# Kernel optimization log

Measured on AMD Instinct MI355X. Metric: run time of the kernel, lower is better.

The kernel has to match this reference:

```python
import jax, jax.numpy as jnp
import numpy as np

N, K, C, S = 32768, 16, 64, 8
EPS = 1e-5

def _bn(x, g, b):
    # BatchNorm1d in training mode: normalize over all axes except channel (last)
    axes = tuple(range(x.ndim - 1))
    m = x.mean(axes, keepdims=True)
    v = x.var(axes, keepdims=True)
    return (x - m) * jax.lax.rsqrt(v + EPS) * g + b

def setup_inputs() -> dict:
    key = jax.random.key(0)
    ks = jax.random.split(key, 24)
    def W(k, i, o):
        return (jax.random.normal(k, (i, o), jnp.float32) * 0.02)
    d = {}
    d['xyz'] = jax.random.normal(ks[0], (N, 3), jnp.float32)
    d['features'] = jax.random.normal(ks[1], (N, C), jnp.float32)
    d['velocities'] = jax.random.normal(ks[2], (N, 1), jnp.float32)
    # q/k/v projections
    d['wq'] = W(ks[3], C, C); d['bq'] = jnp.zeros((C,), jnp.float32)
    d['wk'] = W(ks[4], C, C); d['bk'] = jnp.zeros((C,), jnp.float32)
    d['wv'] = W(ks[5], C, C); d['bv'] = jnp.zeros((C,), jnp.float32)
    # linear_p: Linear(3,3) -> BN(3) -> ReLU -> Linear(3,C)
    d['p1_w'] = W(ks[6], 3, 3); d['p1_b'] = jnp.zeros((3,), jnp.float32)
    d['p_bn_g'] = jnp.ones((3,), jnp.float32); d['p_bn_b'] = jnp.zeros((3,), jnp.float32)
    d['p2_w'] = W(ks[7], 3, C); d['p2_b'] = jnp.zeros((C,), jnp.float32)
    # velocity encoder: Linear(1,1) -> BN(1) -> ReLU -> Linear(1,C)
    d['v1_w'] = W(ks[8], 1, 1); d['v1_b'] = jnp.zeros((1,), jnp.float32)
    d['v_bn_g'] = jnp.ones((1,), jnp.float32); d['v_bn_b'] = jnp.zeros((1,), jnp.float32)
    d['v2_w'] = W(ks[9], 1, C); d['v2_b'] = jnp.zeros((C,), jnp.float32)
    # linear_w: BN(C) -> ReLU -> Linear(C, C//S) -> BN(C//S) -> ReLU -> Linear(C//S, C//S)
    d['w_bn1_g'] = jnp.ones((C,), jnp.float32); d['w_bn1_b'] = jnp.zeros((C,), jnp.float32)
    d['w1_w'] = W(ks[10], C, C // S); d['w1_b'] = jnp.zeros((C // S,), jnp.float32)
    d['w_bn2_g'] = jnp.ones((C // S,), jnp.float32); d['w_bn2_b'] = jnp.zeros((C // S,), jnp.float32)
    d['w2_w'] = W(ks[11], C // S, C // S); d['w2_b'] = jnp.zeros((C // S,), jnp.float32)
    # rho: BN(C) -> ReLU -> Linear(C, C)
    d['rho_bn_g'] = jnp.ones((C,), jnp.float32); d['rho_bn_b'] = jnp.zeros((C,), jnp.float32)
    d['rho_w'] = W(ks[12], C, C); d['rho_b'] = jnp.zeros((C,), jnp.float32)
    # precomputed KNN neighbor indices (coordinate-space and velocity-space)
    d['idx'] = jax.random.randint(ks[13], (N, K), 0, N, jnp.int32)
    d['idx_v'] = jax.random.randint(ks[14], (N, K), 0, N, jnp.int32)
    return d

def reference(xyz, features, velocities, wq, bq, wk, bk, wv, bv,
              p1_w, p1_b, p_bn_g, p_bn_b, p2_w, p2_b,
              v1_w, v1_b, v_bn_g, v_bn_b, v2_w, v2_b,
              w_bn1_g, w_bn1_b, w1_w, w1_b, w_bn2_g, w_bn2_b, w2_w, w2_b,
              rho_bn_g, rho_bn_b, rho_w, rho_b, idx, idx_v):
    x_q = features @ wq + bq                      # [N,C]
    x_k = features @ wk + bk
    x_v = features @ wv + bv
    # queryandgroup: gather neighbors; relative coords prepended for k-path
    p_r = xyz[idx] - xyz[:, None, :]              # [N,K,3]
    x_k_g = x_k[idx]                              # [N,K,C]
    x_v_g = x_v[idx]                              # [N,K,C]
    # positional encoder
    p_enc = jax.nn.relu(_bn(p_r @ p1_w + p1_b, p_bn_g, p_bn_b)) @ p2_w + p2_b   # [N,K,C]
    # velocity encoder (KNN in velocity space)
    v_g = velocities[idx_v]                        # [N,K,1]
    v_enc = jax.nn.relu(_bn(v_g @ v1_w + v1_b, v_bn_g, v_bn_b)) @ v2_w + v2_b   # [N,K,C]
    # subtraction attention scoring
    w = x_k_g - x_q[:, None, :] + (p_enc + v_enc)  # [N,K,C]
    w = jax.nn.relu(_bn(w, w_bn1_g, w_bn1_b)) @ w1_w + w1_b
    w = jax.nn.relu(_bn(w, w_bn2_g, w_bn2_b)) @ w2_w + w2_b   # [N,K,C//S]
    w = jax.nn.softmax(w, axis=1)                  # softmax over neighbors
    # grouped weighted sum with share_planes
    a = (x_v_g + p_enc + v_enc).reshape(N, K, S, C // S)
    out = (a * w[:, :, None, :]).sum(axis=1).reshape(N, C)
    out = out + features
    out = jax.nn.relu(_bn(out, rho_bn_g, rho_bn_b)) @ rho_w + rho_b
    return out
```

## Files before the change

### kernel.cpp

```cpp
#include <hip/hip_runtime.h>

#define NPTS 32768
#define KNN 16
#define CH 64
#define CS 8
#define NKP (NPTS*KNN)
#define EPSBN 1e-5f

#define G1 1024
#define G2 1024
#define G3 1024
#define G4 1024
#define G5 1024

struct EncParams {
  float q00,q01,q02,q10,q11,q12,q20,q21,q22;
  float pb0,pb1,pb2;
  float ps0,ps1,ps2, pt0,pt1,pt2;
  float v1w, v1b, vs, vt;
};

__device__ __forceinline__ EncParams load_enc(const float* __restrict__ p1w, const float* __restrict__ p1b,
                                              const float* __restrict__ v1w, const float* __restrict__ v1b,
                                              const float* __restrict__ stats) {
  EncParams P;
  P.q00=p1w[0]; P.q01=p1w[1]; P.q02=p1w[2];
  P.q10=p1w[3]; P.q11=p1w[4]; P.q12=p1w[5];
  P.q20=p1w[6]; P.q21=p1w[7]; P.q22=p1w[8];
  P.pb0=p1b[0]; P.pb1=p1b[1]; P.pb2=p1b[2];
  P.ps0=stats[0]; P.ps1=stats[1]; P.ps2=stats[2];
  P.pt0=stats[3]; P.pt1=stats[4]; P.pt2=stats[5];
  P.v1w=v1w[0]; P.v1b=v1b[0]; P.vs=stats[6]; P.vt=stats[7];
  return P;
}

__device__ __forceinline__ void enc_scalars(const EncParams& P, const float* __restrict__ xyz,
                                            const float* __restrict__ vel, int m, int mv,
                                            float xn0, float xn1, float xn2,
                                            float& ry0, float& ry1, float& ry2, float& rv) {
  float pr0 = xyz[m*3+0]-xn0, pr1 = xyz[m*3+1]-xn1, pr2 = xyz[m*3+2]-xn2;
  float y0 = pr0*P.q00 + pr1*P.q10 + pr2*P.q20 + P.pb0;
  float y1 = pr0*P.q01 + pr1*P.q11 + pr2*P.q21 + P.pb1;
  float y2 = pr0*P.q02 + pr1*P.q12 + pr2*P.q22 + P.pb2;
  ry0 = fmaxf(y0*P.ps0+P.pt0, 0.f);
  ry1 = fmaxf(y1*P.ps1+P.pt1, 0.f);
  ry2 = fmaxf(y2*P.ps2+P.pt2, 0.f);
  float vr = vel[mv]*P.v1w + P.v1b;
  rv = fmaxf(vr*P.vs+P.vt, 0.f);
}

__global__ __launch_bounds__(256) void k1_qkv_stats(
    const float* __restrict__ feat,
    const float* __restrict__ wq, const float* __restrict__ bq,
    const float* __restrict__ wk, const float* __restrict__ bk,
    const float* __restrict__ wv, const float* __restrict__ bv,
    const float* __restrict__ xyz, const float* __restrict__ vel,
    const float* __restrict__ p1w, const float* __restrict__ p1b,
    const float* __restrict__ v1w, const float* __restrict__ v1b,
    const int* __restrict__ idx, const int* __restrict__ idxv,
    float* __restrict__ xq, float* __restrict__ xk, float* __restrict__ xv,
    float* __restrict__ part1)
{
  __shared__ float4 lw4[3072];
  __shared__ float lf[2048];
  __shared__ float red1[32];
  float* lw = (float*)lw4;
  int tid = threadIdx.x;
  for (int i = tid; i < 3072; i += 256) {
    float4 v;
    if (i < 1024) v = ((const float4*)wq)[i];
    else if (i < 2048) v = ((const float4*)wk)[i-1024];
    else v = ((const float4*)wv)[i-2048];
    lw4[i] = v;
  }
  __syncthreads();
  int lane = tid & 63, wave = tid >> 6;
  int nb = blockIdx.x*32 + wave*8;
  #pragma unroll
  for (int r=0;r<8;r++)
    lf[wave*512 + r*64 + lane] = feat[(nb+r)*64 + lane];
  float aq[8], ak[8], av[8];
  #pragma unroll
  for (int r=0;r<8;r++){ aq[r]=0.f; ak[r]=0.f; av[r]=0.f; }
  for (int i=0;i<64;i++){
    float wqi = lw[i*64+lane];
    float wki = lw[4096+i*64+lane];
    float wvi = lw[8192+i*64+lane];
    #pragma unroll
    for (int r=0;r<8;r++){
      float f = lf[wave*512 + r*64 + i];
      aq[r] += f*wqi; ak[r] += f*wki; av[r] += f*wvi;
    }
  }
  float bql=bq[lane], bkl=bk[lane], bvl=bv[lane];
  #pragma unroll
  for (int r=0;r<8;r++){
    int row = nb + r;
    xq[row*64+lane] = aq[r]+bql;
    xk[row*64+lane] = ak[r]+bkl;
    xv[row*64+lane] = av[r]+bvl;
  }
  float q00=p1w[0],q01=p1w[1],q02=p1w[2],q10=p1w[3],q11=p1w[4],q12=p1w[5],q20=p1w[6],q21=p1w[7],q22=p1w[8];
  float pb0=p1b[0],pb1=p1b[1],pb2=p1b[2];
  float v1w_=v1w[0], v1b_=v1b[0];
  float s0=0,s1=0,s2=0,sv=0,t0=0,t1=0,t2=0,tv=0;
  int gid = blockIdx.x*256 + tid;
  #pragma unroll
  for (int rep=0; rep<2; rep++){
    int p = gid + rep*(G1*256);
    int n = p >> 4;
    int m = idx[p], mv = idxv[p];
    float xn0=xyz[n*3], xn1=xyz[n*3+1], xn2=xyz[n*3+2];
    float pr0=xyz[m*3]-xn0, pr1=xyz[m*3+1]-xn1, pr2=xyz[m*3+2]-xn2;
    float y0 = pr0*q00+pr1*q10+pr2*q20+pb0;
    float y1 = pr0*q01+pr1*q11+pr2*q21+pb1;
    float y2 = pr0*q02+pr1*q12+pr2*q22+pb2;
    float vr = vel[mv]*v1w_ + v1b_;
    s0+=y0; s1+=y1; s2+=y2; sv+=vr;
    t0+=y0*y0; t1+=y1*y1; t2+=y2*y2; tv+=vr*vr;
  }
  #pragma unroll
  for (int msk=1; msk<64; msk<<=1){
    s0 += __shfl_xor(s0,msk); s1 += __shfl_xor(s1,msk); s2 += __shfl_xor(s2,msk); sv += __shfl_xor(sv,msk);
    t0 += __shfl_xor(t0,msk); t1 += __shfl_xor(t1,msk); t2 += __shfl_xor(t2,msk); tv += __shfl_xor(tv,msk);
  }
  if (lane==0){
    red1[wave*8+0]=s0; red1[wave*8+1]=s1; red1[wave*8+2]=s2; red1[wave*8+3]=sv;
    red1[wave*8+4]=t0; red1[wave*8+5]=t1; red1[wave*8+6]=t2; red1[wave*8+7]=tv;
  }
  __syncthreads();
  if (tid < 8){
    float a = red1[tid] + red1[8+tid] + red1[16+tid] + red1[24+tid];
    part1[blockIdx.x*8 + tid] = a;
  }
}

__global__ __launch_bounds__(1024) void r1_finalize(
    const float* __restrict__ P, const float* __restrict__ pg, const float* __restrict__ pb,
    const float* __restrict__ vg, const float* __restrict__ vb, float* __restrict__ stats)
{
  constexpr int COLG = 2, NSL = 1024/COLG, ITER = G1/NSL;
  __shared__ float4 red[1024];
  int t = threadIdx.x; int cg = t % COLG, sl = t / COLG;
  float4 acc = make_float4(0.f,0.f,0.f,0.f);
  const float4* P4 = (const float4*)P;
  #pragma unroll
  for (int j=0;j<ITER;j++){
    int i = sl + j*NSL;
    float4 v = P4[i*COLG + cg];
    acc.x+=v.x; acc.y+=v.y; acc.z+=v.z; acc.w+=v.w;
  }
  red[t] = acc; __syncthreads();
  for (int off = NSL/2; off>0; off>>=1){
    if (sl < off){
      float4 o = red[(sl+off)*COLG + cg];
      acc.x+=o.x; acc.y+=o.y; acc.z+=o.z; acc.w+=o.w;
      red[sl*COLG + cg] = acc;
    }
    __syncthreads();
  }
  if (t<4){
    float s = ((float*)red)[t];
    float q = ((float*)red)[4+t];
    float inv = 1.f/(float)NKP;
    float mean=s*inv, var=q*inv-mean*mean;
    float g = (t<3)? pg[t]:vg[0];
    float b = (t<3)? pb[t]:vb[0];
    float sc = g*rsqrtf(var+EPSBN);
    float sh = b - mean*sc;
    if (t<3){ stats[t]=sc; stats[3+t]=sh; } else { stats[6]=sc; stats[7]=sh; }
  }
}

__global__ __launch_bounds__(256) void k1b_renc(
    const float* __restrict__ xyz, const float* __restrict__ vel,
    const float* __restrict__ p1w, const float* __restrict__ p1b,
    const float* __restrict__ v1w, const float* __restrict__ v1b,
    const int* __restrict__ idx, const int* __restrict__ idxv,
    const float* __restrict__ stats, float* __restrict__ renc)
{
  EncParams P = load_enc(p1w,p1b,v1w,v1b,stats);
  int p = blockIdx.x*256 + threadIdx.x;
  int n = p >> 4;
  int m = idx[p], mv = idxv[p];
  float ry0,ry1,ry2,rv;
  enc_scalars(P, xyz, vel, m, mv, xyz[n*3], xyz[n*3+1], xyz[n*3+2], ry0,ry1,ry2,rv);
  ((float4*)renc)[p] = make_float4(ry0,ry1,ry2,rv);
}

template<int NB, int NCH>
__global__ __launch_bounds__(1024) void finalize_bn_t(
    const float* __restrict__ P, float inv,
    const float* __restrict__ g, const float* __restrict__ b,
    float* __restrict__ oscale, float* __restrict__ oshift)
{
  constexpr int COLS = 2*NCH;
  constexpr int COLG = COLS/4;
  constexpr int NSL  = 1024/COLG;
  constexpr int ITER = NB/NSL;
  __shared__ float4 red[1024];
  int t = threadIdx.x; int cg = t % COLG, sl = t / COLG;
  float4 acc = make_float4(0.f,0.f,0.f,0.f);
  const float4* P4 = (const float4*)P;
  #pragma unroll 8
  for (int j=0;j<ITER;j++){
    int i = sl + j*NSL;
    float4 v = P4[i*COLG + cg];
    acc.x+=v.x; acc.y+=v.y; acc.z+=v.z; acc.w+=v.w;
  }
  red[t] = acc; __syncthreads();
  for (int off = NSL/2; off>0; off>>=1){
    if (sl < off){
      float4 o = red[(sl+off)*COLG + cg];
      acc.x+=o.x; acc.y+=o.y; acc.z+=o.z; acc.w+=o.w;
      red[sl*COLG + cg] = acc;
    }
    __syncthreads();
  }
  if (t < NCH){
    float s = ((float*)red)[t];
    float q = ((float*)red)[NCH + t];
    float mean=s*inv, var=q*inv-mean*mean;
    float sc=g[t]*rsqrtf(var+EPSBN);
    oscale[t]=sc; oshift[t]=b[t]-mean*sc;
  }
}

__global__ __launch_bounds__(256) void k2_wstats(
    const int* __restrict__ idx, const float* __restrict__ renc,
    const float* __restrict__ p2w, const float* __restrict__ p2b,
    const float* __restrict__ v2w, const float* __restrict__ v2b,
    const float* __restrict__ xq, const float* __restrict__ xk,
    float* __restrict__ part2)
{
  int tid = threadIdx.x;
  int lane = tid & 63, wave = tid >> 6;
  float A = p2w[lane], B = p2w[64+lane], C2 = p2w[128+lane];
  float D = v2w[lane], E = p2b[lane] + v2b[lane];
  const float4* renc4 = (const float4*)renc;
  float sum=0.f, ssq=0.f;
  int gw = blockIdx.x*4 + wave;
  for (int n0 = gw; n0 < NPTS; n0 += G2*4){
    int nu = __builtin_amdgcn_readfirstlane(n0);
    float xqc = xq[nu*64+lane];
    #pragma unroll 4
    for (int k=0;k<KNN;k++){
      int pu = nu*KNN + k;
      int m = idx[pu];
      float4 rr = renc4[pu];
      float e = rr.x*A + rr.y*B + rr.z*C2 + rr.w*D + E;
      float w = xk[m*64+lane] - xqc + e;
      sum += w; ssq += w*w;
    }
  }
  __shared__ float rs[4][64], rq[4][64];
  rs[wave][lane]=sum; rq[wave][lane]=ssq;
  __syncthreads();
  if (tid < 64){
    float s = rs[0][tid]+rs[1][tid]+rs[2][tid]+rs[3][tid];
    float q = rq[0][tid]+rq[1][tid]+rq[2][tid]+rq[3][tid];
    part2[blockIdx.x*128 + tid] = s;
    part2[blockIdx.x*128 + 64 + tid] = q;
  }
}

__global__ __launch_bounds__(256) void k3_w1(
    const float* __restrict__ p2w, const float* __restrict__ p2b,
    const float* __restrict__ v2w, const float* __restrict__ v2b,
    const float* __restrict__ w1w, const float* __restrict__ w1b,
    const int* __restrict__ idx, const float* __restrict__ renc,
    const float* __restrict__ xq, const float* __restrict__ xk,
    const float* __restrict__ stats,
    float* __restrict__ w1o, float* __restrict__ part3)
{
  __shared__ __attribute__((aligned(16))) float coef[64*20];
  __shared__ float rs[256], rq[256];
  int tid=threadIdx.x;
  if (tid < 64){
    int c = tid;
    int slot = ((c&7)<<3) | (c>>3);
    float* cf = &coef[slot*20];
    cf[0]=p2w[c]; cf[1]=p2w[64+c]; cf[2]=p2w[128+c];
    cf[3]=v2w[c]; cf[4]=p2b[c]+v2b[c];
    cf[5]=stats[8+c]; cf[6]=stats[72+c];
    #pragma unroll
    for (int j=0;j<8;j++) cf[7+j]=w1w[c*8+j];
    #pragma unroll
    for (int j=15;j<20;j++) cf[j]=0.f;
  }
  __syncthreads();
  int lane=tid&63, wave=tid>>6;
  int sl = lane&7, sp = lane>>3;
  float w1b_l = w1b[sl];
  const float4* renc4=(const float4*)renc;
  const float4* xk4=(const float4*)xk;
  const float4* xq4=(const float4*)xq;
  float ssum=0.f, sqq=0.f;
  int gw = blockIdx.x*4 + wave;
  for (int it = gw; it < NKP/32; it += G3*4){
    int pbase = it*32 + sp*4;
    int n = pbase >> 4;
    int4 mi = *(const int4*)&idx[pbase];
    float4 rr0 = renc4[pbase+0], rr1 = renc4[pbase+1],
           rr2 = renc4[pbase+2], rr3 = renc4[pbase+3];
    float4 xqa = xq4[n*16 + sl*2], xqb = xq4[n*16 + sl*2 + 1];
    float xqv[8] = {xqa.x,xqa.y,xqa.z,xqa.w, xqb.x,xqb.y,xqb.z,xqb.w};
    float xkv[4][8];
    {
      int mm[4] = {mi.x, mi.y, mi.z, mi.w};
      #pragma unroll
      for (int u=0;u<4;u++){
        float4 a = xk4[mm[u]*16 + sl*2], b = xk4[mm[u]*16 + sl*2 + 1];
        xkv[u][0]=a.x; xkv[u][1]=a.y; xkv[u][2]=a.z; xkv[u][3]=a.w;
        xkv[u][4]=b.x; xkv[u][5]=b.y; xkv[u][6]=b.z; xkv[u][7]=b.w;
      }
    }
    float h[4][8];
    #pragma unroll
    for (int u=0;u<4;u++)
      #pragma unroll
      for (int j=0;j<8;j++) h[u][j]=0.f;
    float4 rrs[4] = {rr0,rr1,rr2,rr3};
    #pragma unroll
    for (int r=0;r<8;r++){
      const float* cf = &coef[(r*8+sl)*20];
      float4 ca = *(const float4*)(cf+0);
      float4 cb = *(const float4*)(cf+4);
      float4 cc = *(const float4*)(cf+8);
      float4 cd = *(const float4*)(cf+12);
      #pragma unroll
      for (int u=0;u<4;u++){
        float e = rrs[u].x*ca.x + rrs[u].y*ca.y + rrs[u].z*ca.z + rrs[u].w*ca.w + cb.x;
        float w = xkv[u][r] - xqv[r] + e;
        float rw = fmaxf(w*cb.y + cb.z, 0.f);
        h[u][0] += rw*cb.w; h[u][1] += rw*cc.x; h[u][2] += rw*cc.y; h[u][3] += rw*cc.z;
        h[u][4] += rw*cc.w; h[u][5] += rw*cd.x; h[u][6] += rw*cd.y; h[u][7] += rw*cd.z;
      }
    }
    bool k1b_ = (sl&1)==0, k2b = (sl&2)==0, k4b = (sl&4)==0;
    #pragma unroll
    for (int u=0;u<4;u++){
      float a0 = k1b_? h[u][0]:h[u][1], o0 = k1b_? h[u][1]:h[u][0];
      float a1 = k1b_? h[u][2]:h[u][3], o1 = k1b_? h[u][3]:h[u][2];
      float a2 = k1b_? h[u][4]:h[u][5], o2 = k1b_? h[u][5]:h[u][4];
      float a3 = k1b_? h[u][6]:h[u][7], o3 = k1b_? h[u][7]:h[u][6];
      float g0 = a0 + __shfl_xor(o0,1);
      float g1 = a1 + __shfl_xor(o1,1);
      float g2 = a2 + __shfl_xor(o2,1);
      float g3 = a3 + __shfl_xor(o3,1);
      float b0 = k2b? g0:g1, p0 = k2b? g1:g0;
      float b1 = k2b? g2:g3, p1 = k2b? g3:g2;
      float f0 = b0 + __shfl_xor(p0,2);
      float f1 = b1 + __shfl_xor(p1,2);
      float c0 = k4b? f0:f1, q0 = k4b? f1:f0;
      float S = c0 + __shfl_xor(q0,4);
      float o = S + w1b_l;
      w1o[(pbase+u)*8 + sl] = o;
      ssum += o; sqq += o*o;
    }
  }
  rs[tid]=ssum; rq[tid]=sqq;
  __syncthreads();
  if (tid < 8){
    float s=0.f,q=0.f;
    #pragma unroll 8
    for (int i=0;i<32;i++){ s+=rs[i*8+tid]; q+=rq[i*8+tid]; }
    part3[blockIdx.x*16 + tid] = s;
    part3[blockIdx.x*16 + 8 + tid] = q;
  }
}

__global__ __launch_bounds__(256) void k4_agg(
    const float* __restrict__ feat,
    const float* __restrict__ p2w, const float* __restrict__ p2b,
    const float* __restrict__ v2w, const float* __restrict__ v2b,
    const float* __restrict__ w2w, const float* __restrict__ w2b,
    const int* __restrict__ idx, const float* __restrict__ renc,
    const float* __restrict__ xv, const float* __restrict__ w1o,
    const float* __restrict__ stats,
    float* __restrict__ outpre, float* __restrict__ part4)
{
  __shared__ float sm_s[4][16][8];
  __shared__ float rs[4][64], rq[4][64];
  int tid=threadIdx.x, lane=tid&63, wave=tid>>6;
  int kq = lane & 15, jh = lane >> 4;
  float s2[8], t2[8];
  #pragma unroll
  for (int i=0;i<8;i++){ s2[i]=stats[136+i]; t2[i]=stats[144+i]; }
  float w2c0[8], w2c1[8];
  #pragma unroll
  for (int i=0;i<8;i++){ w2c0[i]=w2w[i*8+jh]; w2c1[i]=w2w[i*8+jh+4]; }
  float w2b0=w2b[jh], w2b1=w2b[jh+4];
  float A=p2w[lane], B=p2w[64+lane], C2=p2w[128+lane], D=v2w[lane], E=p2b[lane]+v2b[lane];
  int j = lane & 7;
  const float4* renc4 = (const float4*)renc;
  float sr=0.f, sq2=0.f;
  int gw = blockIdx.x*4 + wave;
  for (int n0 = gw; n0 < NPTS; n0 += G4*4){
    int nu = __builtin_amdgcn_readfirstlane(n0);
    const float* w1p = &w1o[(nu*KNN + kq)*8];
    float4 wa = *(const float4*)w1p;
    float4 wb = *(const float4*)(w1p+4);
    float r0 = fmaxf(wa.x*s2[0]+t2[0],0.f);
    float r1 = fmaxf(wa.y*s2[1]+t2[1],0.f);
    float r2 = fmaxf(wa.z*s2[2]+t2[2],0.f);
    float r3 = fmaxf(wa.w*s2[3]+t2[3],0.f);
    float r4 = fmaxf(wb.x*s2[4]+t2[4],0.f);
    float r5 = fmaxf(wb.y*s2[5]+t2[5],0.f);
    float r6 = fmaxf(wb.z*s2[6]+t2[6],0.f);
    float r7 = fmaxf(wb.w*s2[7]+t2[7],0.f);
    float g0 = r0*w2c0[0]+r1*w2c0[1]+r2*w2c0[2]+r3*w2c0[3]
             + r4*w2c0[4]+r5*w2c0[5]+r6*w2c0[6]+r7*w2c0[7] + w2b0;
    float g1 = r0*w2c1[0]+r1*w2c1[1]+r2*w2c1[2]+r3*w2c1[3]
             + r4*w2c1[4]+r5*w2c1[5]+r6*w2c1[6]+r7*w2c1[7] + w2b1;
    float m0=g0, m1=g1;
    #pragma unroll
    for (int msk=1; msk<16; msk<<=1){
      m0 = fmaxf(m0, __shfl_xor(m0,msk));
      m1 = fmaxf(m1, __shfl_xor(m1,msk));
    }
    float e0=__expf(g0-m0), e1=__expf(g1-m1);
    float d0=e0, d1=e1;
    #pragma unroll
    for (int msk=1; msk<16; msk<<=1){ d0 += __shfl_xor(d0,msk); d1 += __shfl_xor(d1,msk); }
    sm_s[wave][kq][jh]   = e0/d0;
    sm_s[wave][kq][jh+4] = e1/d1;
    __syncthreads();
    float acc=0.f;
    #pragma unroll 4
    for (int k=0;k<KNN;k++){
      int pu = nu*KNN+k;
      int m = idx[pu];
      float4 rr = renc4[pu];
      float e = rr.x*A + rr.y*B + rr.z*C2 + rr.w*D + E;
      acc += (xv[m*64+lane] + e) * sm_s[wave][k][j];
    }
    float o = acc + feat[nu*64+lane];
    outpre[nu*64+lane] = o;
    sr += o; sq2 += o*o;
    __syncthreads();
  }
  rs[wave][lane]=sr; rq[wave][lane]=sq2;
  __syncthreads();
  if (tid<64){
    float s=rs[0][tid]+rs[1][tid]+rs[2][tid]+rs[3][tid];
    float q=rq[0][tid]+rq[1][tid]+rq[2][tid]+rq[3][tid];
    part4[blockIdx.x*128+tid]=s;
    part4[blockIdx.x*128+64+tid]=q;
  }
}

__global__ __launch_bounds__(256) void k5_rho(
    const float* __restrict__ outpre, const float* __restrict__ stats,
    const float* __restrict__ rhow, const float* __restrict__ rhob,
    float* __restrict__ out)
{
  __shared__ float4 lw4[1024];
  __shared__ float lf[2048];
  float* lw = (float*)lw4;
  int tid=threadIdx.x;
  for (int i=tid;i<1024;i+=256) lw4[i] = ((const float4*)rhow)[i];
  __syncthreads();
  int lane=tid&63, wave=tid>>6;
  int nb = blockIdx.x*32 + wave*8;
  float scl = stats[152+lane], sft = stats[216+lane];
  #pragma unroll
  for (int r=0;r<8;r++){
    float a = outpre[(nb+r)*64+lane];
    lf[wave*512 + r*64 + lane] = fmaxf(a*scl+sft, 0.f);
  }
  float acc[8];
  #pragma unroll
  for (int r=0;r<8;r++) acc[r]=0.f;
  for (int i=0;i<64;i++){
    float w_ = lw[i*64+lane];
    #pragma unroll
    for (int r=0;r<8;r++) acc[r] += lf[wave*512+r*64+i]*w_;
  }
  float bl = rhob[lane];
  #pragma unroll
  for (int r=0;r<8;r++) out[(nb+r)*64+lane] = acc[r] + bl;
}

extern "C" void kernel_launch(void* const* d_in, const int* in_sizes, int n_in,
                              void* d_out, int out_size, void* d_ws, size_t ws_size,
                              hipStream_t stream) {
  const float* xyz  = (const float*)d_in[0];
  const float* feat = (const float*)d_in[1];
  const float* vel  = (const float*)d_in[2];
  const float* wq   = (const float*)d_in[3];  const float* bq = (const float*)d_in[4];
  const float* wk   = (const float*)d_in[5];  const float* bk = (const float*)d_in[6];
  const float* wv   = (const float*)d_in[7];  const float* bv = (const float*)d_in[8];
  const float* p1w  = (const float*)d_in[9];  const float* p1b = (const float*)d_in[10];
  const float* pbg  = (const float*)d_in[11]; const float* pbb = (const float*)d_in[12];
  const float* p2w  = (const float*)d_in[13]; const float* p2b = (const float*)d_in[14];
  const float* v1w  = (const float*)d_in[15]; const float* v1b = (const float*)d_in[16];
  const float* vbg  = (const float*)d_in[17]; const float* vbb = (const float*)d_in[18];
  const float* v2w  = (const float*)d_in[19]; const float* v2b = (const float*)d_in[20];
  const float* wbn1g= (const float*)d_in[21]; const float* wbn1b= (const float*)d_in[22];
  const float* w1w  = (const float*)d_in[23]; const float* w1b = (const float*)d_in[24];
  const float* wbn2g= (const float*)d_in[25]; const float* wbn2b= (const float*)d_in[26];
  const float* w2w  = (const float*)d_in[27]; const float* w2b = (const float*)d_in[28];
  const float* rbg  = (const float*)d_in[29]; const float* rbb = (const float*)d_in[30];
  const float* rhow = (const float*)d_in[31]; const float* rhob = (const float*)d_in[32];
  const int* idx    = (const int*)d_in[33];
  const int* idxv   = (const int*)d_in[34];

  float* ws = (float*)d_ws;
  float* xq     = ws;
  float* xk     = xq + (size_t)NPTS*CH;
  float* xv     = xk + (size_t)NPTS*CH;
  float* w1o    = xv + (size_t)NPTS*CH;
  float* outpre = w1o + (size_t)NKP*CS;
  float* renc   = outpre + (size_t)NPTS*CH;
  float* part1  = renc + (size_t)NKP*4;
  float* part2  = part1 + G1*8;
  float* part3  = part2 + G2*128;
  float* part4  = part3 + G3*16;
  float* stats  = part4 + G4*128;

  k1_qkv_stats<<<dim3(G1), dim3(256), 0, stream>>>(
      feat, wq,bq,wk,bk,wv,bv, xyz, vel, p1w,p1b,v1w,v1b, idx, idxv, xq,xk,xv, part1);
  r1_finalize<<<dim3(1), dim3(1024), 0, stream>>>(part1, pbg,pbb, vbg,vbb, stats);
  k1b_renc<<<dim3(NKP/256), dim3(256), 0, stream>>>(
      xyz, vel, p1w,p1b, v1w,v1b, idx, idxv, stats, renc);
  k2_wstats<<<dim3(G2), dim3(256), 0, stream>>>(
      idx, renc, p2w,p2b,v2w,v2b, xq, xk, part2);
  finalize_bn_t<G2,64><<<dim3(1), dim3(1024), 0, stream>>>(
      part2, 1.f/(float)NKP, wbn1g, wbn1b, stats+8, stats+72);
  k3_w1<<<dim3(G3), dim3(256), 0, stream>>>(
      p2w,p2b,v2w,v2b, w1w,w1b, idx, renc, xq, xk, stats, w1o, part3);
  finalize_bn_t<G3,8><<<dim3(1), dim3(1024), 0, stream>>>(
      part3, 1.f/(float)NKP, wbn2g, wbn2b, stats+136, stats+144);
  k4_agg<<<dim3(G4), dim3(256), 0, stream>>>(
      feat, p2w,p2b,v2w,v2b, w2w,w2b, idx, renc, xv, w1o, stats, outpre, part4);
  finalize_bn_t<G4,64><<<dim3(1), dim3(1024), 0, stream>>>(
      part4, 1.f/(float)NPTS, rbg, rbb, stats+152, stats+216);
  k5_rho<<<dim3(G5), dim3(256), 0, stream>>>(outpre, stats, rhow, rhob, (float*)d_out);

  (void)in_sizes; (void)n_in; (void)out_size; (void)ws_size;
}
```

Baseline: 151.0 us.

## Use DPP reductions, vectorized LDS feature reads, larger grids, drop agg barriers

Doubles the grid sizes of the stats, w1 and aggregation kernels. Replaces the shuffle-based butterfly reductions in k3 and the k4 softmax with DPP row operations, remapping output channel slots to match the DPP lane pattern. Vectorizes the shared-memory feature reads in the two 64x64 matmul kernels as float4. Replaces the __syncthreads in the k4 aggregation loop with compiler memory barriers, on the assumption that each wave only touches its own shared slice. This adds risk of an intra-wave LDS ordering error and of a mistake in the channel remapping.

```diff
diff --git a/kernel.cpp b/kernel.cpp
--- a/kernel.cpp
+++ b/kernel.cpp
@@ -8,10 +8,25 @@
 #define EPSBN 1e-5f
 
 #define G1 1024
-#define G2 1024
-#define G3 1024
-#define G4 1024
+#define G2 2048
+#define G3 2048
+#define G4 2048
 #define G5 1024
+
+template<int CTRL>
+__device__ __forceinline__ float dppf(float x){
+  int r = __builtin_amdgcn_update_dpp(0, __float_as_int(x), CTRL, 0xf, 0xf, true);
+  return __int_as_float(r);
+}
+__device__ __forceinline__ float dpp_sum16(float x){
+  x += dppf<0xB1>(x); x += dppf<0x4E>(x); x += dppf<0x141>(x); x += dppf<0x140>(x);
+  return x;
+}
+__device__ __forceinline__ float dpp_max16(float x){
+  x = fmaxf(x, dppf<0xB1>(x)); x = fmaxf(x, dppf<0x4E>(x));
+  x = fmaxf(x, dppf<0x141>(x)); x = fmaxf(x, dppf<0x140>(x));
+  return x;
+}
 
 struct EncParams {
   float q00,q01,q02,q10,q11,q12,q20,q21,q22;
@@ -61,8 +76,8 @@
     float* __restrict__ xq, float* __restrict__ xk, float* __restrict__ xv,
     float* __restrict__ part1)
 {
-  __shared__ float4 lw4[3072];
-  __shared__ float lf[2048];
+  __shared__ __attribute__((aligned(16))) float4 lw4[3072];
+  __shared__ __attribute__((aligned(16))) float lf[2048];
   __shared__ float red1[32];
   float* lw = (float*)lw4;
   int tid = threadIdx.x;
@@ -82,14 +97,20 @@
   float aq[8], ak[8], av[8];
   #pragma unroll
   for (int r=0;r<8;r++){ aq[r]=0.f; ak[r]=0.f; av[r]=0.f; }
-  for (int i=0;i<64;i++){
-    float wqi = lw[i*64+lane];
-    float wki = lw[4096+i*64+lane];
-    float wvi = lw[8192+i*64+lane];
-    #pragma unroll
-    for (int r=0;r<8;r++){
-      float f = lf[wave*512 + r*64 + i];
-      aq[r] += f*wqi; ak[r] += f*wki; av[r] += f*wvi;
+  for (int i=0;i<64;i+=4){
+    float4 fr[8];
+    #pragma unroll
+    for (int r=0;r<8;r++) fr[r] = *(const float4*)&lf[wave*512 + r*64 + i];
+    #pragma unroll
+    for (int ii=0;ii<4;ii++){
+      float wqi = lw[(i+ii)*64+lane];
+      float wki = lw[4096+(i+ii)*64+lane];
+      float wvi = lw[8192+(i+ii)*64+lane];
+      #pragma unroll
+      for (int r=0;r<8;r++){
+        float f = ii==0?fr[r].x: ii==1?fr[r].y: ii==2?fr[r].z: fr[r].w;
+        aq[r] += f*wqi; ak[r] += f*wki; av[r] += f*wvi;
+      }
     }
   }
   float bql=bq[lane], bkl=bk[lane], bvl=bv[lane];
@@ -291,7 +312,9 @@
   __syncthreads();
   int lane=tid&63, wave=tid>>6;
   int sl = lane&7, sp = lane>>3;
-  float w1b_l = w1b[sl];
+  bool p4 = (sl&4)==0, p1 = (sl&1)==0, p2 = (sl&2)==0;
+  int jmap = (sl&4) | ((sl&1)<<1) | ((sl&2)>>1);
+  float w1b_l = w1b[jmap];
   const float4* renc4=(const float4*)renc;
   const float4* xk4=(const float4*)xk;
   const float4* xq4=(const float4*)xq;
@@ -301,8 +324,7 @@
     int pbase = it*32 + sp*4;
     int n = pbase >> 4;
     int4 mi = *(const int4*)&idx[pbase];
-    float4 rr0 = renc4[pbase+0], rr1 = renc4[pbase+1],
-           rr2 = renc4[pbase+2], rr3 = renc4[pbase+3];
+    float4 rrs[4] = {renc4[pbase+0], renc4[pbase+1], renc4[pbase+2], renc4[pbase+3]};
     float4 xqa = xq4[n*16 + sl*2], xqb = xq4[n*16 + sl*2 + 1];
     float xqv[8] = {xqa.x,xqa.y,xqa.z,xqa.w, xqb.x,xqb.y,xqb.z,xqb.w};
     float xkv[4][8];
@@ -320,7 +342,6 @@
     for (int u=0;u<4;u++)
       #pragma unroll
       for (int j=0;j<8;j++) h[u][j]=0.f;
-    float4 rrs[4] = {rr0,rr1,rr2,rr3};
     #pragma unroll
     for (int r=0;r<8;r++){
       const float* cf = &coef[(r*8+sl)*20];
@@ -337,29 +358,21 @@
         h[u][4] += rw*cc.w; h[u][5] += rw*cd.x; h[u][6] += rw*cd.y; h[u][7] += rw*cd.z;
       }
     }
-    bool k1b_ = (sl&1)==0, k2b = (sl&2)==0, k4b = (sl&4)==0;
     #pragma unroll
     for (int u=0;u<4;u++){
-      float a0 = k1b_? h[u][0]:h[u][1], o0 = k1b_? h[u][1]:h[u][0];
-      float a1 = k1b_? h[u][2]:h[u][3], o1 = k1b_? h[u][3]:h[u][2];
-      float a2 = k1b_? h[u][4]:h[u][5], o2 = k1b_? h[u][5]:h[u][4];
-      float a3 = k1b_? h[u][6]:h[u][7], o3 = k1b_? h[u][7]:h[u][6];
-      float g0 = a0 + __shfl_xor(o0,1);
-      float g1 = a1 + __shfl_xor(o1,1);
-      float g2 = a2 + __shfl_xor(o2,1);
-      float g3 = a3 + __shfl_xor(o3,1);
-      float b0 = k2b? g0:g1, p0 = k2b? g1:g0;
-      float b1 = k2b? g2:g3, p1 = k2b? g3:g2;
-      float f0 = b0 + __shfl_xor(p0,2);
-      float f1 = b1 + __shfl_xor(p1,2);
-      float c0 = k4b? f0:f1, q0 = k4b? f1:f0;
-      float S = c0 + __shfl_xor(q0,4);
+      float g0 = (p4? h[u][0]:h[u][4]) + dppf<0x141>(p4? h[u][4]:h[u][0]);
+      float g1 = (p4? h[u][1]:h[u][5]) + dppf<0x141>(p4? h[u][5]:h[u][1]);
+      float g2 = (p4? h[u][2]:h[u][6]) + dppf<0x141>(p4? h[u][6]:h[u][2]);
+      float g3 = (p4? h[u][3]:h[u][7]) + dppf<0x141>(p4? h[u][7]:h[u][3]);
+      float f0 = (p1? g0:g2) + dppf<0xB1>(p1? g2:g0);
+      float f1 = (p1? g1:g3) + dppf<0xB1>(p1? g3:g1);
+      float S  = (p2? f0:f1) + dppf<0x4E>(p2? f1:f0);
       float o = S + w1b_l;
-      w1o[(pbase+u)*8 + sl] = o;
+      w1o[(pbase+u)*8 + jmap] = o;
       ssum += o; sqq += o*o;
     }
   }
-  rs[tid]=ssum; rq[tid]=sqq;
+  rs[(tid & ~7) | jmap]=ssum; rq[(tid & ~7) | jmap]=sqq;
   __syncthreads();
   if (tid < 8){
     float s=0.f,q=0.f;
@@ -413,19 +426,12 @@
              + r4*w2c0[4]+r5*w2c0[5]+r6*w2c0[6]+r7*w2c0[7] + w2b0;
     float g1 = r0*w2c1[0]+r1*w2c1[1]+r2*w2c1[2]+r3*w2c1[3]
              + r4*w2c1[4]+r5*w2c1[5]+r6*w2c1[6]+r7*w2c1[7] + w2b1;
-    float m0=g0, m1=g1;
-    #pragma unroll
-    for (int msk=1; msk<16; msk<<=1){
-      m0 = fmaxf(m0, __shfl_xor(m0,msk));
-      m1 = fmaxf(m1, __shfl_xor(m1,msk));
-    }
+    float m0 = dpp_max16(g0), m1 = dpp_max16(g1);
     float e0=__expf(g0-m0), e1=__expf(g1-m1);
-    float d0=e0, d1=e1;
-    #pragma unroll
-    for (int msk=1; msk<16; msk<<=1){ d0 += __shfl_xor(d0,msk); d1 += __shfl_xor(d1,msk); }
+    float d0 = dpp_sum16(e0), d1 = dpp_sum16(e1);
     sm_s[wave][kq][jh]   = e0/d0;
     sm_s[wave][kq][jh+4] = e1/d1;
-    __syncthreads();
+    __asm__ __volatile__("" ::: "memory");
     float acc=0.f;
     #pragma unroll 4
     for (int k=0;k<KNN;k++){
@@ -438,7 +444,7 @@
     float o = acc + feat[nu*64+lane];
     outpre[nu*64+lane] = o;
     sr += o; sq2 += o*o;
-    __syncthreads();
+    __asm__ __volatile__("" ::: "memory");
   }
   rs[wave][lane]=sr; rq[wave][lane]=sq2;
   __syncthreads();
@@ -455,8 +461,8 @@
     const float* __restrict__ rhow, const float* __restrict__ rhob,
     float* __restrict__ out)
 {
-  __shared__ float4 lw4[1024];
-  __shared__ float lf[2048];
+  __shared__ __attribute__((aligned(16))) float4 lw4[1024];
+  __shared__ __attribute__((aligned(16))) float lf[2048];
   float* lw = (float*)lw4;
   int tid=threadIdx.x;
   for (int i=tid;i<1024;i+=256) lw4[i] = ((const float4*)rhow)[i];
@@ -472,10 +478,19 @@
   float acc[8];
   #pragma unroll
   for (int r=0;r<8;r++) acc[r]=0.f;
-  for (int i=0;i<64;i++){
-    float w_ = lw[i*64+lane];
-    #pragma unroll
-    for (int r=0;r<8;r++) acc[r] += lf[wave*512+r*64+i]*w_;
+  for (int i=0;i<64;i+=4){
+    float4 fr[8];
+    #pragma unroll
+    for (int r=0;r<8;r++) fr[r] = *(const float4*)&lf[wave*512 + r*64 + i];
+    #pragma unroll
+    for (int ii=0;ii<4;ii++){
+      float w_ = lw[(i+ii)*64+lane];
+      #pragma unroll
+      for (int r=0;r<8;r++){
+        float f = ii==0?fr[r].x: ii==1?fr[r].y: ii==2?fr[r].z: fr[r].w;
+        acc[r] += f*w_;
+      }
+    }
   }
   float bl = rhob[lane];
   #pragma unroll
@@ -515,9 +530,9 @@
   float* renc   = outpre + (size_t)NPTS*CH;
   float* part1  = renc + (size_t)NKP*4;
   float* part2  = part1 + G1*8;
-  float* part3  = part2 + G2*128;
+  float* part3  = part2 + (size_t)G2*128;
   float* part4  = part3 + G3*16;
-  float* stats  = part4 + G4*128;
+  float* stats  = part4 + (size_t)G4*128;
 
   k1_qkv_stats<<<dim3(G1), dim3(256), 0, stream>>>(
       feat, wq,bq,wk,bk,wv,bv, xyz, vel, p1w,p1b,v1w,v1b, idx, idxv, xq,xk,xv, part1);
```

Result: no change. 153.7 us (+1.7%).
